# Optimization experiments

Measured on AMD Instinct MI355X. Metric: run time of the kernel, lower is better.

The kernel has to match this reference:

```python
import jax, jax.numpy as jnp
import numpy as np

D = 128          # cfg_node_encoding_dim
N_NODES = 300000
EPS = 1e-9


def setup_inputs() -> dict:
    key = jax.random.key(0)
    ks = jax.random.split(key, 10)
    inp = {
        "occ_ngram3": jax.random.normal(ks[0], (250000, 3, D), dtype=jnp.float32),
        "idx_ngram3": jax.random.randint(ks[1], (250000, 3), 0, N_NODES, dtype=jnp.int64),
        "occ_ngram5": jax.random.normal(ks[2], (200000, 5, D), dtype=jnp.float32),
        "idx_ngram5": jax.random.randint(ks[3], (200000, 5), 0, N_NODES, dtype=jnp.int64),
        "previous_cfg_nodes_encodings": jax.random.normal(ks[4], (N_NODES, D), dtype=jnp.float32),
        # learned params: attention key projection + GRU-like gate
        "attn_W": jax.random.normal(ks[5], (D, D), dtype=jnp.float32) / np.sqrt(D),
        "attn_b": jnp.zeros((D,), dtype=jnp.float32),
        "gate_W": jax.random.normal(ks[6], (2 * D, D), dtype=jnp.float32) / np.sqrt(2 * D),
        "gate_b": jnp.zeros((D,), dtype=jnp.float32),
        "nr_cfg_nodes": N_NODES,
    }
    return inp


def _scatter_attn_gate(occ3, occ5, prev, attn_W, attn_b, gate_W, gate_b, idx3, idx5, n_nodes):
    # flatten(0,1) + cat over sorted ngram lengths -> [E, D] values, [E] indices
    vals = jnp.concatenate([occ3.reshape(-1, D), occ5.reshape(-1, D)], axis=0)
    idx = jnp.concatenate([idx3.reshape(-1), idx5.reshape(-1)], axis=0)

    # scatter-attention keyed on previous node encodings
    keys = prev @ attn_W + attn_b                        # [N, D]
    scores = jnp.einsum('ed,ed->e', vals, keys[idx]) / jnp.sqrt(jnp.asarray(D, vals.dtype))
    seg_max = jax.ops.segment_max(scores, idx, num_segments=n_nodes)   # -inf for empty segs
    ex = jnp.exp(scores - seg_max[idx])
    denom = jax.ops.segment_sum(ex, idx, num_segments=n_nodes)
    probs = ex / (denom[idx] + EPS)                      # segment softmax [E]
    agg = jax.ops.segment_sum(probs[:, None] * vals, idx, num_segments=n_nodes)  # [N, D]

    # GRU-like gate: z = sigmoid(W [prev; update]); new = z*update + (1-z)*prev
    z = jax.nn.sigmoid(jnp.concatenate([prev, agg], axis=-1) @ gate_W + gate_b)
    return z * agg + (1.0 - z) * prev


def reference(occ_ngram3, idx_ngram3, occ_ngram5, idx_ngram5,
              previous_cfg_nodes_encodings, attn_W, attn_b, gate_W, gate_b,
              nr_cfg_nodes):
    return _scatter_attn_gate(occ_ngram3, occ_ngram5, previous_cfg_nodes_encodings,
                              attn_W, attn_b, gate_W, gate_b,
                              idx_ngram3, idx_ngram5, nr_cfg_nodes)
```

## Files before the change

kernel.cpp:

```cpp
#include <hip/hip_runtime.h>
#include <math.h>

#define D 128
#define EPSF 1e-9f

typedef __bf16 bf16x8 __attribute__((ext_vector_type(8)));
typedef float  f32x4  __attribute__((ext_vector_type(4)));
typedef float  f32x2  __attribute__((ext_vector_type(2)));

static __device__ __forceinline__ float bf2f(unsigned short h) {
    union { unsigned int u; float f; } c; c.u = ((unsigned int)h) << 16;
    return c.f;
}
static __device__ __forceinline__ unsigned short f2bf(float f) {
    union { float f; unsigned int u; } c; c.f = f;
    unsigned int u = c.u + 0x7fffu + ((c.u >> 16) & 1u);
    return (unsigned short)(u >> 16);
}

__global__ __launch_bounds__(256) void transpose_w_kernel(
    const float* __restrict__ attn_W, const float* __restrict__ gate_W,
    __bf16* __restrict__ wta, __bf16* __restrict__ wtg)
{
    int i = blockIdx.x * 256 + threadIdx.x;
    if (i < 128 * 128) {
        int k = i >> 7, n = i & 127;
        wta[n * 128 + k] = (__bf16)attn_W[i];
    }
    if (i < 256 * 128) {
        int k = i >> 7, n = i & 127;
        wtg[n * 256 + k] = (__bf16)gate_W[i];
    }
}

__global__ __launch_bounds__(256) void keys_mfma_kernel(
    const float* __restrict__ prev, const __bf16* __restrict__ wta,
    const float* __restrict__ attn_b, unsigned short* __restrict__ keysb, int N)
{
    const int lane = threadIdx.x & 63;
    const int wid  = threadIdx.x >> 6;
    const int m0 = (blockIdx.x * 4 + wid) * 16;
    if (m0 >= N) return;
    const int lm = lane & 15;
    const int lg = lane >> 4;

    int arow = m0 + lm; if (arow >= N) arow = m0;
    const float* ap = prev + (size_t)arow * D + lg * 8;

    f32x4 acc[8] = {};
    #pragma unroll
    for (int kk = 0; kk < 4; ++kk) {
        float4 a0 = *(const float4*)(ap + kk * 32);
        float4 a1 = *(const float4*)(ap + kk * 32 + 4);
        bf16x8 af;
        af[0] = (__bf16)a0.x; af[1] = (__bf16)a0.y; af[2] = (__bf16)a0.z; af[3] = (__bf16)a0.w;
        af[4] = (__bf16)a1.x; af[5] = (__bf16)a1.y; af[6] = (__bf16)a1.z; af[7] = (__bf16)a1.w;
        const int k0 = kk * 32;
        #pragma unroll
        for (int t = 0; t < 8; ++t) {
            bf16x8 bf_ = *(const bf16x8*)(wta + (size_t)(t * 16 + lm) * 128 + k0 + lg * 8);
            acc[t] = __builtin_amdgcn_mfma_f32_16x16x32_bf16(af, bf_, acc[t], 0, 0, 0);
        }
    }
    __bf16* kb = (__bf16*)keysb;
    #pragma unroll
    for (int t = 0; t < 8; ++t) {
        float bcol = attn_b[t * 16 + lm];
        #pragma unroll
        for (int r = 0; r < 4; ++r) {
            int row = m0 + lg * 4 + r;
            if (row < N)
                kb[(size_t)row * D + t * 16 + lm] = (__bf16)(acc[t][r] + bcol);
        }
    }
}

__global__ __launch_bounds__(256) void hist_kernel(
    const int* __restrict__ idx3, const int* __restrict__ idx5,
    int* __restrict__ cnt, int* __restrict__ rank, int E3, int E)
{
    int e = blockIdx.x * 256 + threadIdx.x;
    if (e >= E) return;
    int n = (e < E3) ? idx3[e] : idx5[e - E3];
    rank[e] = atomicAdd(&cnt[n], 1);
}

__global__ __launch_bounds__(256) void scan1_kernel(
    const int* __restrict__ cnt, int* __restrict__ row_start,
    int* __restrict__ bsum, int N)
{
    __shared__ int tsum[256];
    const int t = threadIdx.x;
    const int base = blockIdx.x * 1024;
    const int i0 = base + t * 4;
    int v0 = 0, v1 = 0, v2 = 0, v3 = 0;
    if (i0 + 0 < N) v0 = cnt[i0 + 0];
    if (i0 + 1 < N) v1 = cnt[i0 + 1];
    if (i0 + 2 < N) v2 = cnt[i0 + 2];
    if (i0 + 3 < N) v3 = cnt[i0 + 3];
    int s = v0 + v1 + v2 + v3;
    tsum[t] = s;
    __syncthreads();
    int val = s;
    for (int off = 1; off < 256; off <<= 1) {
        int tmp = (t >= off) ? tsum[t - off] : 0;
        __syncthreads();
        val += tmp; tsum[t] = val;
        __syncthreads();
    }
    int excl = val - s;
    if (i0 + 0 < N) row_start[i0 + 0] = excl;            excl += v0;
    if (i0 + 1 < N) row_start[i0 + 1] = excl;            excl += v1;
    if (i0 + 2 < N) row_start[i0 + 2] = excl;            excl += v2;
    if (i0 + 3 < N) row_start[i0 + 3] = excl;
    if (t == 255) bsum[blockIdx.x] = val;
}

__global__ __launch_bounds__(1024) void scan2_kernel(int* __restrict__ bsum, int nb)
{
    __shared__ int sh[1024];
    const int t = threadIdx.x;
    int v = (t < nb) ? bsum[t] : 0;
    sh[t] = v;
    __syncthreads();
    int val = v;
    for (int off = 1; off < 1024; off <<= 1) {
        int tmp = (t >= off) ? sh[t - off] : 0;
        __syncthreads();
        val += tmp; sh[t] = val;
        __syncthreads();
    }
    if (t < nb) bsum[t] = val - v;
}

__global__ __launch_bounds__(256) void scan3_kernel(
    int* __restrict__ row_start, const int* __restrict__ bsum, int N, int E)
{
    int i = blockIdx.x * 256 + threadIdx.x;
    if (i < N)       row_start[i] += bsum[i >> 10];
    else if (i == N) row_start[N] = E;
}

__global__ __launch_bounds__(256) void scatter_kernel(
    const int* __restrict__ idx3, const int* __restrict__ idx5,
    const int* __restrict__ row_start, const int* __restrict__ rank,
    int* __restrict__ edge_ids, int E3, int E)
{
    int e = blockIdx.x * 256 + threadIdx.x;
    if (e >= E) return;
    int n = (e < E3) ? idx3[e] : idx5[e - E3];
    edge_ids[row_start[n] + rank[e]] = e;
}

__global__ __launch_bounds__(256) void agg_kernel(
    const float* __restrict__ occ3, const float* __restrict__ occ5,
    const unsigned short* __restrict__ keysb,
    const int* __restrict__ row_start, const int* __restrict__ edge_ids,
    unsigned int* __restrict__ aggb, int E3, int N)
{
    const int lane = threadIdx.x & 63;
    const int wid  = threadIdx.x >> 6;
    const int n = blockIdx.x * 4 + wid;
    if (n >= N) return;

    unsigned int kp = ((const unsigned int*)keysb)[(size_t)n * (D / 2) + lane];
    float kx = bf2f((unsigned short)(kp & 0xffffu));
    float ky = bf2f((unsigned short)(kp >> 16));

    const int rs = row_start[n];
    const int re = row_start[n + 1];
    const float scale = 0.0883883476483184f;

    float ax = 0.f, ay = 0.f, den = 0.f;

    for (int base = rs; base < re; base += 64) {
        const int left = re - base;
        const int cnt = left < 64 ? left : 64;
        int myid = (lane < cnt) ? edge_ids[base + lane] : 0;

        for (int j0 = 0; j0 < cnt; j0 += 8) {
            f32x2 v[8];
            #pragma unroll
            for (int j = 0; j < 8; ++j) {
                int e = __shfl(myid, j0 + j);
                const f32x2* vp = (e < E3)
                    ? (const f32x2*)(occ3 + (size_t)e * D)
                    : (const f32x2*)(occ5 + (size_t)(e - E3) * D);
                v[j] = __builtin_nontemporal_load(&vp[lane]);
            }
            float s[8];
            #pragma unroll
            for (int j = 0; j < 8; ++j)
                s[j] = v[j][0] * kx + v[j][1] * ky;
            #pragma unroll
            for (int sh = 32; sh >= 1; sh >>= 1) {
                #pragma unroll
                for (int j = 0; j < 8; ++j)
                    s[j] += __shfl_xor(s[j], sh);
            }
            #pragma unroll
            for (int j = 0; j < 8; ++j) {
                float ex = (j0 + j < cnt) ? __expf(s[j] * scale) : 0.f;
                den += ex;
                ax = fmaf(ex, v[j][0], ax);
                ay = fmaf(ex, v[j][1], ay);
            }
        }
    }

    float inv = 1.0f / (den + EPSF);
    unsigned int pack = (unsigned int)f2bf(ax * inv)
                      | ((unsigned int)f2bf(ay * inv) << 16);
    aggb[(size_t)n * (D / 2) + lane] = pack;
}

__global__ __launch_bounds__(256) void gate_mfma_kernel(
    const float* __restrict__ prev, const __bf16* __restrict__ aggb,
    const __bf16* __restrict__ wtg, const float* __restrict__ gate_b,
    float* __restrict__ out, int N)
{
    const int lane = threadIdx.x & 63;
    const int wid  = threadIdx.x >> 6;
    const int m0 = (blockIdx.x * 4 + wid) * 16;
    if (m0 >= N) return;
    const int lm = lane & 15;
    const int lg = lane >> 4;

    int arow = m0 + lm; if (arow >= N) arow = m0;
    const float*  aprev = prev + (size_t)arow * D + lg * 8;
    const __bf16* aagg  = aggb + (size_t)arow * D + lg * 8;

    f32x4 acc[8] = {};
    #pragma unroll
    for (int kk = 0; kk < 4; ++kk) {
        float4 a0 = *(const float4*)(aprev + kk * 32);
        float4 a1 = *(const float4*)(aprev + kk * 32 + 4);
        bf16x8 af;
        af[0] = (__bf16)a0.x; af[1] = (__bf16)a0.y; af[2] = (__bf16)a0.z; af[3] = (__bf16)a0.w;
        af[4] = (__bf16)a1.x; af[5] = (__bf16)a1.y; af[6] = (__bf16)a1.z; af[7] = (__bf16)a1.w;
        const int k0 = kk * 32;
        #pragma unroll
        for (int t = 0; t < 8; ++t) {
            bf16x8 bf_ = *(const bf16x8*)(wtg + (size_t)(t * 16 + lm) * 256 + k0 + lg * 8);
            acc[t] = __builtin_amdgcn_mfma_f32_16x16x32_bf16(af, bf_, acc[t], 0, 0, 0);
        }
    }
    #pragma unroll
    for (int kk = 0; kk < 4; ++kk) {
        bf16x8 af = *(const bf16x8*)(aagg + kk * 32);
        const int k0 = 128 + kk * 32;
        #pragma unroll
        for (int t = 0; t < 8; ++t) {
            bf16x8 bf_ = *(const bf16x8*)(wtg + (size_t)(t * 16 + lm) * 256 + k0 + lg * 8);
            acc[t] = __builtin_amdgcn_mfma_f32_16x16x32_bf16(af, bf_, acc[t], 0, 0, 0);
        }
    }

    const unsigned short* aggu = (const unsigned short*)aggb;
    #pragma unroll
    for (int t = 0; t < 8; ++t) {
        float bcol = gate_b[t * 16 + lm];
        #pragma unroll
        for (int r = 0; r < 4; ++r) {
            int row = m0 + lg * 4 + r;
            if (row < N) {
                size_t off = (size_t)row * D + t * 16 + lm;
                float c = acc[t][r] + bcol;
                float z = 1.0f / (1.0f + __expf(-c));
                float a = bf2f(aggu[off]);
                float p = prev[off];
                __builtin_nontemporal_store(fmaf(z, a - p, p), &out[off]);
            }
        }
    }
}

extern "C" void kernel_launch(void* const* d_in, const int* in_sizes, int n_in,
                              void* d_out, int out_size, void* d_ws, size_t ws_size,
                              hipStream_t stream)
{
    const float* occ3   = (const float*)d_in[0];
    const int*   idx3   = (const int*)d_in[1];
    const float* occ5   = (const float*)d_in[2];
    const int*   idx5   = (const int*)d_in[3];
    const float* prev   = (const float*)d_in[4];
    const float* attn_W = (const float*)d_in[5];
    const float* attn_b = (const float*)d_in[6];
    const float* gate_W = (const float*)d_in[7];
    const float* gate_b = (const float*)d_in[8];

    const int N  = in_sizes[4] / D;
    const int E3 = in_sizes[1];
    const int E5 = in_sizes[3];
    const int E  = E3 + E5;

    unsigned short* keysb = (unsigned short*)d_ws;
    unsigned int*   aggb  = (unsigned int*)(keysb + (size_t)N * D);
    int* row_start = (int*)((unsigned short*)aggb + (size_t)N * D);
    int* cnt       = row_start + (N + 1);
    int* bsum      = cnt + N;
    int* rank      = bsum + 1025;
    int* edge_ids  = rank + E;
    __bf16* wta    = (__bf16*)(edge_ids + E);
    __bf16* wtg    = wta + 128 * 128;

    float* out = (float*)d_out;

    (void)hipMemsetAsync(cnt, 0, (size_t)N * sizeof(int), stream);

    transpose_w_kernel<<<128, 256, 0, stream>>>(attn_W, gate_W, wta, wtg);

    const int nb = (N + 1023) / 1024;
    hist_kernel   <<<(E + 255) / 256, 256, 0, stream>>>(idx3, idx5, cnt, rank, E3, E);
    scan1_kernel  <<<nb, 256, 0, stream>>>(cnt, row_start, bsum, N);
    scan2_kernel  <<<1, 1024, 0, stream>>>(bsum, nb);
    scan3_kernel  <<<(N + 256) / 256, 256, 0, stream>>>(row_start, bsum, N, E);
    scatter_kernel<<<(E + 255) / 256, 256, 0, stream>>>(idx3, idx5, row_start, rank, edge_ids, E3, E);

    keys_mfma_kernel<<<(N + 63) / 64, 256, 0, stream>>>(prev, wta, attn_b, keysb, N);

    agg_kernel<<<(N + 3) / 4, 256, 0, stream>>>(occ3, occ5, keysb, row_start, edge_ids, aggb, E3, N);

    gate_mfma_kernel<<<(N + 63) / 64, 256, 0, stream>>>(prev, (const __bf16*)aggb, wtg, gate_b, out, N);
}
```

Before: 707.1 us.

## Fuse weight transpose with histogram and stage MFMA epilogues through LDS

Merges the weight-transpose kernel and the edge histogram kernel into one launch, with the first 128 blocks doing the transpose and the rest doing the atomic counting. The keys and gate kernels now write their MFMA accumulators into a per-wave shared-memory tile, then read them back row-contiguously. This allows vectorized 4-wide global stores of keys, and vectorized loads of prev and agg plus 16-byte nontemporal stores in the gate epilogue. The cost is 32 KB of LDS per block, which may limit occupancy, and an extra LDS round trip.

Result: faster. 667.8 us (-5.6%).

```diff
diff --git a/kernel.cpp b/kernel.cpp
--- a/kernel.cpp
+++ b/kernel.cpp
@@ -18,18 +18,28 @@
     return (unsigned short)(u >> 16);
 }
 
-__global__ __launch_bounds__(256) void transpose_w_kernel(
+__global__ __launch_bounds__(256) void hist_transpose_kernel(
     const float* __restrict__ attn_W, const float* __restrict__ gate_W,
-    __bf16* __restrict__ wta, __bf16* __restrict__ wtg)
-{
-    int i = blockIdx.x * 256 + threadIdx.x;
-    if (i < 128 * 128) {
-        int k = i >> 7, n = i & 127;
-        wta[n * 128 + k] = (__bf16)attn_W[i];
-    }
-    if (i < 256 * 128) {
-        int k = i >> 7, n = i & 127;
-        wtg[n * 256 + k] = (__bf16)gate_W[i];
+    __bf16* __restrict__ wta, __bf16* __restrict__ wtg,
+    const int* __restrict__ idx3, const int* __restrict__ idx5,
+    int* __restrict__ cnt, int* __restrict__ rank, int E3, int E)
+{
+    int b = blockIdx.x;
+    if (b < 128) {
+        int i = b * 256 + threadIdx.x;
+        if (i < 128 * 128) {
+            int k = i >> 7, n = i & 127;
+            wta[n * 128 + k] = (__bf16)attn_W[i];
+        }
+        {
+            int k = i >> 7, n = i & 127;
+            wtg[n * 256 + k] = (__bf16)gate_W[i];
+        }
+    } else {
+        int e = (b - 128) * 256 + threadIdx.x;
+        if (e >= E) return;
+        int n = (e < E3) ? idx3[e] : idx5[e - E3];
+        rank[e] = atomicAdd(&cnt[n], 1);
     }
 }
 
@@ -37,6 +47,7 @@
     const float* __restrict__ prev, const __bf16* __restrict__ wta,
     const float* __restrict__ attn_b, unsigned short* __restrict__ keysb, int N)
 {
+    __shared__ float stg[4][16 * D];
     const int lane = threadIdx.x & 63;
     const int wid  = threadIdx.x >> 6;
     const int m0 = (blockIdx.x * 4 + wid) * 16;
@@ -62,27 +73,28 @@
             acc[t] = __builtin_amdgcn_mfma_f32_16x16x32_bf16(af, bf_, acc[t], 0, 0, 0);
         }
     }
-    __bf16* kb = (__bf16*)keysb;
+
+    float* kw = stg[wid];
     #pragma unroll
     for (int t = 0; t < 8; ++t) {
         float bcol = attn_b[t * 16 + lm];
         #pragma unroll
-        for (int r = 0; r < 4; ++r) {
-            int row = m0 + lg * 4 + r;
-            if (row < N)
-                kb[(size_t)row * D + t * 16 + lm] = (__bf16)(acc[t][r] + bcol);
-        }
-    }
-}
-
-__global__ __launch_bounds__(256) void hist_kernel(
-    const int* __restrict__ idx3, const int* __restrict__ idx5,
-    int* __restrict__ cnt, int* __restrict__ rank, int E3, int E)
-{
-    int e = blockIdx.x * 256 + threadIdx.x;
-    if (e >= E) return;
-    int n = (e < E3) ? idx3[e] : idx5[e - E3];
-    rank[e] = atomicAdd(&cnt[n], 1);
+        for (int r = 0; r < 4; ++r)
+            kw[(lg * 4 + r) * D + t * 16 + lm] = acc[t][r] + bcol;
+    }
+    #pragma unroll
+    for (int q = 0; q < 8; ++q) {
+        int idx = q * 64 + lane;
+        int ro = idx >> 5;
+        int co = (idx & 31) * 4;
+        int row = m0 + ro;
+        if (row < N) {
+            f32x4 c = *(const f32x4*)&kw[ro * D + co];
+            ushort4 o;
+            o.x = f2bf(c[0]); o.y = f2bf(c[1]); o.z = f2bf(c[2]); o.w = f2bf(c[3]);
+            *(ushort4*)(keysb + (size_t)row * D + co) = o;
+        }
+    }
 }
 
 __global__ __launch_bounds__(256) void scan1_kernel(
@@ -219,6 +231,7 @@
     const __bf16* __restrict__ wtg, const float* __restrict__ gate_b,
     float* __restrict__ out, int N)
 {
+    __shared__ float stg[4][16 * D];
     const int lane = threadIdx.x & 63;
     const int wid  = threadIdx.x >> 6;
     const int m0 = (blockIdx.x * 4 + wid) * 16;
@@ -256,21 +269,33 @@
         }
     }
 
-    const unsigned short* aggu = (const unsigned short*)aggb;
+    float* zw = stg[wid];
     #pragma unroll
     for (int t = 0; t < 8; ++t) {
         float bcol = gate_b[t * 16 + lm];
         #pragma unroll
-        for (int r = 0; r < 4; ++r) {
-            int row = m0 + lg * 4 + r;
-            if (row < N) {
-                size_t off = (size_t)row * D + t * 16 + lm;
-                float c = acc[t][r] + bcol;
-                float z = 1.0f / (1.0f + __expf(-c));
-                float a = bf2f(aggu[off]);
-                float p = prev[off];
-                __builtin_nontemporal_store(fmaf(z, a - p, p), &out[off]);
-            }
+        for (int r = 0; r < 4; ++r)
+            zw[(lg * 4 + r) * D + t * 16 + lm] = acc[t][r] + bcol;
+    }
+    const unsigned short* aggu = (const unsigned short*)aggb;
+    #pragma unroll
+    for (int q = 0; q < 8; ++q) {
+        int idx = q * 64 + lane;
+        int ro = idx >> 5;
+        int co = (idx & 31) * 4;
+        int row = m0 + ro;
+        if (row < N) {
+            size_t off = (size_t)row * D + co;
+            f32x4 c = *(const f32x4*)&zw[ro * D + co];
+            f32x4 p = *(const f32x4*)(prev + off);
+            ushort4 a4 = *(const ushort4*)(aggu + off);
+            f32x4 o;
+            float z;
+            z = 1.0f / (1.0f + __expf(-c[0])); o[0] = fmaf(z, bf2f(a4.x) - p[0], p[0]);
+            z = 1.0f / (1.0f + __expf(-c[1])); o[1] = fmaf(z, bf2f(a4.y) - p[1], p[1]);
+            z = 1.0f / (1.0f + __expf(-c[2])); o[2] = fmaf(z, bf2f(a4.z) - p[2], p[2]);
+            z = 1.0f / (1.0f + __expf(-c[3])); o[3] = fmaf(z, bf2f(a4.w) - p[3], p[3]);
+            __builtin_nontemporal_store(o, (f32x4*)(out + off));
         }
     }
 }
@@ -308,10 +333,11 @@
 
     (void)hipMemsetAsync(cnt, 0, (size_t)N * sizeof(int), stream);
 
-    transpose_w_kernel<<<128, 256, 0, stream>>>(attn_W, gate_W, wta, wtg);
+    const int hblocks = (E + 255) / 256;
+    hist_transpose_kernel<<<128 + hblocks, 256, 0, stream>>>(
+        attn_W, gate_W, wta, wtg, idx3, idx5, cnt, rank, E3, E);
 
     const int nb = (N + 1023) / 1024;
-    hist_kernel   <<<(E + 255) / 256, 256, 0, stream>>>(idx3, idx5, cnt, rank, E3, E);
     scan1_kernel  <<<nb, 256, 0, stream>>>(cnt, row_start, bsum, N);
     scan2_kernel  <<<1, 1024, 0, stream>>>(bsum, nb);
     scan3_kernel  <<<(N + 256) / 256, 256, 0, stream>>>(row_start, bsum, N, E);
```
